# Kernel optimization log

Hardware: AMD Instinct MI355X
Metric: run time of the kernel (lower is better)

The kernel has to match this reference:

```python
import jax, jax.numpy as jnp
import numpy as np
import math

CHANNELS = 512
N_HEADS = 8
K_CH = CHANNELS // N_HEADS            # 64 per-head dim
ROPE_D = int(K_CH * 0.5)              # 32 dims get RoPE, rest pass through
BASE = 10000


def _rope(x):
    # x: [b, h, t, dk]; rotate first ROPE_D dims (half-split style, matching the torch module)
    d = ROPE_D
    t = x.shape[2]
    theta = 1.0 / (BASE ** (jnp.arange(0, d, 2, dtype=jnp.float32) / d))      # [d/2]
    ang = jnp.arange(t, dtype=jnp.float32)[:, None] * theta[None, :]          # [t, d/2]
    ang = jnp.concatenate([ang, ang], axis=-1)                                # [t, d]
    cos = jnp.cos(ang)[None, None, :, :].astype(x.dtype)
    sin = jnp.sin(ang)[None, None, :, :].astype(x.dtype)
    x_rope, x_pass = x[..., :d], x[..., d:]
    neg_half = jnp.concatenate([-x_rope[..., d // 2:], x_rope[..., :d // 2]], axis=-1)
    return jnp.concatenate([x_rope * cos + neg_half * sin, x_pass], axis=-1)


def _split_heads(y):
    # [b, (h c), t] -> [b, h, t, c]
    b, _, t = y.shape
    return y.reshape(b, N_HEADS, K_CH, t).transpose(0, 1, 3, 2)


def setup_inputs() -> dict:
    key = jax.random.key(0)
    ks = jax.random.split(key, 10)
    B, T = 8, 1024
    w_scale = 1.0 / math.sqrt(CHANNELS)
    return {
        "x": jax.random.normal(ks[0], (B, CHANNELS, T), jnp.float32),
        "c": jax.random.normal(ks[1], (B, CHANNELS, T), jnp.float32),
        "Wq": jax.random.normal(ks[2], (CHANNELS, CHANNELS), jnp.float32) * w_scale,
        "bq": jax.random.normal(ks[3], (CHANNELS,), jnp.float32) * 0.02,
        "Wk": jax.random.normal(ks[4], (CHANNELS, CHANNELS), jnp.float32) * w_scale,
        "bk": jax.random.normal(ks[5], (CHANNELS,), jnp.float32) * 0.02,
        "Wv": jax.random.normal(ks[6], (CHANNELS, CHANNELS), jnp.float32) * w_scale,
        "bv": jax.random.normal(ks[7], (CHANNELS,), jnp.float32) * 0.02,
        "Wo": jax.random.normal(ks[8], (CHANNELS, CHANNELS), jnp.float32) * w_scale,
        "bo": jax.random.normal(ks[9], (CHANNELS,), jnp.float32) * 0.02,
    }


def reference(x, c, Wq, bq, Wk, bk, Wv, bv, Wo, bo):
    # 1x1 Conv1d == per-timestep linear over channels
    q = jnp.einsum('oc,bct->bot', Wq, x) + bq[None, :, None]
    k = jnp.einsum('oc,bct->bot', Wk, c) + bk[None, :, None]
    v = jnp.einsum('oc,bct->bot', Wv, c) + bv[None, :, None]

    q = _rope(_split_heads(q))            # [b,h,t,ck]
    k = _rope(_split_heads(k))            # [b,h,s,ck]
    v = _split_heads(v)                   # [b,h,s,ck]

    scale = 1.0 / math.sqrt(K_CH)
    scores = jnp.einsum('bhtc,bhsc->bhts', q, k) * scale
    p_attn = jax.nn.softmax(scores, axis=-1)       # dropout p=0 -> identity
    out = jnp.einsum('bhts,bhsc->bhtc', p_attn, v)

    b, _, t, _ = out.shape
    out = out.transpose(0, 1, 3, 2).reshape(b, CHANNELS, t)   # [b, (h c), t]
    return jnp.einsum('oc,bct->bot', Wo, out) + bo[None, :, None]
```

## Files before the change

### kernel.cpp

```cpp
#include <hip/hip_runtime.h>

typedef __bf16 bf16x8 __attribute__((ext_vector_type(8)));
typedef float  f32x4  __attribute__((ext_vector_type(4)));

__device__ __forceinline__ unsigned short f2bf(float f){
    union { float f; unsigned u; } v; v.f = f;
    v.u += 0x7fffu + ((v.u >> 16) & 1u);
    return (unsigned short)(v.u >> 16);
}
__device__ __forceinline__ unsigned short f2bf_trunc(float f){
    union { float f; unsigned u; } v; v.f = f;
    return (unsigned short)(v.u >> 16);
}
__device__ __forceinline__ void gl2lds16(const unsigned short* g, unsigned short* l){
    __builtin_amdgcn_global_load_lds(
        (const __attribute__((address_space(1))) void*)g,
        (__attribute__((address_space(3))) void*)l, 16, 0, 0);
}

__global__ __launch_bounds__(256) void cvt_bf16_4(const float* __restrict__ w0, const float* __restrict__ w1,
                                                  const float* __restrict__ w2, const float* __restrict__ w3,
                                                  unsigned short* __restrict__ o0, unsigned short* __restrict__ o1,
                                                  unsigned short* __restrict__ o2, unsigned short* __restrict__ o3){
    const float* in; unsigned short* out;
    switch (blockIdx.y){
        case 0: in = w0; out = o0; break;
        case 1: in = w1; out = o1; break;
        case 2: in = w2; out = o2; break;
        default: in = w3; out = o3; break;
    }
    int i = (blockIdx.x * 256 + threadIdx.x) * 4;
    float4 v = *(const float4*)(in + i);
    ushort4 o; o.x = f2bf(v.x); o.y = f2bf(v.y); o.z = f2bf(v.z); o.w = f2bf(v.w);
    *(ushort4*)(out + i) = o;
}

__global__ __launch_bounds__(256) void transpose_cvt(const float* __restrict__ x, const float* __restrict__ c,
                                                     unsigned short* __restrict__ xt, unsigned short* __restrict__ ct){
    __shared__ float tile[64][72];
    const int z = blockIdx.z;
    const float* in = (z < 8) ? x : c;
    unsigned short* out = (z < 8) ? xt : ct;
    const int b = z & 7;
    const int t0 = blockIdx.x * 64, c0 = blockIdx.y * 64;
    const int tid = threadIdx.x;
    {
        int r = tid >> 2, q = (tid & 3) * 16;
        const float* src = in + ((size_t)b * 512 + c0 + r) * 1024 + t0 + q;
        *(float4*)&tile[r][q + 0]  = ((const float4*)src)[0];
        *(float4*)&tile[r][q + 4]  = ((const float4*)src)[1];
        *(float4*)&tile[r][q + 8]  = ((const float4*)src)[2];
        *(float4*)&tile[r][q + 12] = ((const float4*)src)[3];
    }
    __syncthreads();
    {
        int tr = tid >> 2, cj = (tid & 3) * 16;
        unsigned pw[8];
        #pragma unroll
        for (int j = 0; j < 8; j++){
            unsigned lo = f2bf(tile[cj + 2*j    ][tr]);
            unsigned hi = f2bf(tile[cj + 2*j + 1][tr]);
            pw[j] = lo | (hi << 16);
        }
        unsigned short* dst = out + ((size_t)b * 1024 + t0 + tr) * 512 + c0 + cj;
        uint4 o0 = {pw[0], pw[1], pw[2], pw[3]};
        uint4 o1 = {pw[4], pw[5], pw[6], pw[7]};
        ((uint4*)dst)[0] = o0;
        ((uint4*)dst)[1] = o1;
    }
}

__device__ __forceinline__ void gemm_mainloop(const unsigned short* __restrict__ A,
                                              const unsigned short* __restrict__ Bm,
                                              unsigned short* a_s, unsigned short* b_s,
                                              int m0, int n0, int tid, f32x4 acc[4][4]){
    const int wave = tid >> 6, lane = tid & 63;
    const int l15 = lane & 15, l4 = lane >> 4;
    const int mw = (wave >> 1) * 64, nw = (wave & 1) * 64;
    const int r8 = lane >> 3, c8l = lane & 7;
    const int csw = (c8l ^ r8) * 8;
    const int rp = l15 & 7;

    for (int k0 = 0; k0 < 512; k0 += 64){
        #pragma unroll
        for (int i = 0; i < 4; i++){
            int rg = i * 4 + wave;
            int row = rg * 8 + r8;
            gl2lds16(A  + (size_t)(m0 + row) * 512 + k0 + csw, a_s + rg * 512);
            gl2lds16(Bm + (size_t)(n0 + row) * 512 + k0 + csw, b_s + rg * 512);
        }
        __syncthreads();
        #pragma unroll
        for (int kk = 0; kk < 2; kk++){
            bf16x8 af[4], bfr[4];
            #pragma unroll
            for (int mt = 0; mt < 4; mt++)
                af[mt] = *(const bf16x8*)&a_s[(mw + mt*16 + l15)*64 + (((kk*4) + l4) ^ rp)*8];
            #pragma unroll
            for (int ct = 0; ct < 4; ct++)
                bfr[ct] = *(const bf16x8*)&b_s[(nw + ct*16 + l15)*64 + (((kk*4) + l4) ^ rp)*8];
            #pragma unroll
            for (int mt = 0; mt < 4; mt++)
                #pragma unroll
                for (int ct = 0; ct < 4; ct++)
                    acc[mt][ct] = __builtin_amdgcn_mfma_f32_16x16x32_bf16(
                        af[mt], bfr[ct], acc[mt][ct], 0, 0, 0);
        }
        __syncthreads();
    }
}

__global__ __launch_bounds__(256) void qkv_gemm(const unsigned short* __restrict__ xt,
                                                const unsigned short* __restrict__ ct,
                                                const unsigned short* __restrict__ wq,
                                                const unsigned short* __restrict__ wk,
                                                const unsigned short* __restrict__ wv,
                                                const float* __restrict__ bq_,
                                                const float* __restrict__ bk_,
                                                const float* __restrict__ bv_,
                                                unsigned short* __restrict__ qt,
                                                unsigned short* __restrict__ kt,
                                                unsigned short* __restrict__ vct){
    __shared__ unsigned short a_s[128*64];
    __shared__ unsigned short b_s[128*64];
    const int z = blockIdx.y, bid = blockIdx.x;
    const unsigned short *A, *Bm;
    int m0, n0;
    if (z == 0){ A = xt; Bm = wq; m0 = (bid >> 2)*128; n0 = (bid & 3)*128; }
    else if (z == 1){ A = ct; Bm = wk; m0 = (bid >> 2)*128; n0 = (bid & 3)*128; }
    else { A = wv; Bm = ct; m0 = (bid & 3)*128; n0 = (bid >> 2)*128; }
    const int tid = threadIdx.x;
    const int wave = tid >> 6, lane = tid & 63;
    const int l15 = lane & 15, l4 = lane >> 4;
    const int mw = (wave >> 1) * 64, nw = (wave & 1) * 64;
    const f32x4 vzero = {0.f, 0.f, 0.f, 0.f};
    f32x4 acc[4][4];
    #pragma unroll
    for (int i = 0; i < 4; i++)
        #pragma unroll
        for (int j = 0; j < 4; j++) acc[i][j] = vzero;

    gemm_mainloop(A, Bm, a_s, b_s, m0, n0, tid, acc);

    if (z < 2){
        unsigned short* out = (z == 0) ? qt : kt;
        const float* bias = (z == 0) ? bq_ : bk_;
        const float oscale = (z == 0) ? 0.125f : 1.0f;
        float bv4[4];
        #pragma unroll
        for (int ct2 = 0; ct2 < 4; ct2++) bv4[ct2] = bias[n0 + nw + ct2*16 + l15];
        const float theta = __powf(10000.0f, -(float)l15 * (1.0f / 16.0f));
        #pragma unroll
        for (int mt = 0; mt < 4; mt++){
            #pragma unroll
            for (int r = 0; r < 4; r++){
                int row = m0 + mw + mt*16 + l4*4 + r;
                int t = row & 1023;
                float v[4];
                #pragma unroll
                for (int ct2 = 0; ct2 < 4; ct2++) v[ct2] = acc[mt][ct2][r] + bv4[ct2];
                float sn, cn;
                __sincosf((float)t * theta, &sn, &cn);
                float r0 = v[0] * cn - v[1] * sn;
                float r1 = v[1] * cn + v[0] * sn;
                v[0] = r0; v[1] = r1;
                #pragma unroll
                for (int ct2 = 0; ct2 < 4; ct2++)
                    out[(size_t)row * 512 + n0 + nw + ct2*16 + l15] = f2bf(v[ct2] * oscale);
            }
        }
    } else {
        #pragma unroll
        for (int mt = 0; mt < 4; mt++){
            #pragma unroll
            for (int r = 0; r < 4; r++){
                int row = m0 + mw + mt*16 + l4*4 + r;
                float bb = bv_[row];
                #pragma unroll
                for (int ct2 = 0; ct2 < 4; ct2++){
                    int n = n0 + nw + ct2*16 + l15;
                    size_t oaddr = (size_t)(n >> 10) * 524288 + (size_t)row * 1024 + (n & 1023);
                    vct[oaddr] = f2bf(acc[mt][ct2][r] + bb);
                }
            }
        }
    }
}

__global__ __launch_bounds__(256) void gemm_o(const unsigned short* __restrict__ wo,
                                              const unsigned short* __restrict__ attnT,
                                              const float* __restrict__ bo,
                                              float* __restrict__ out){
    __shared__ unsigned short a_s[128*64];
    __shared__ unsigned short b_s[128*64];
    const int m0 = blockIdx.x * 128, n0 = blockIdx.y * 128;
    const int tid = threadIdx.x;
    const int wave = tid >> 6, lane = tid & 63;
    const int l15 = lane & 15, l4 = lane >> 4;
    const int mw = (wave >> 1) * 64, nw = (wave & 1) * 64;
    const f32x4 vzero = {0.f, 0.f, 0.f, 0.f};
    f32x4 acc[4][4];
    #pragma unroll
    for (int i = 0; i < 4; i++)
        #pragma unroll
        for (int j = 0; j < 4; j++) acc[i][j] = vzero;

    gemm_mainloop(wo, attnT, a_s, b_s, m0, n0, tid, acc);

    #pragma unroll
    for (int mt = 0; mt < 4; mt++){
        #pragma unroll
        for (int r = 0; r < 4; r++){
            int row = m0 + mw + mt*16 + l4*4 + r;
            float bb = bo[row];
            #pragma unroll
            for (int ct2 = 0; ct2 < 4; ct2++){
                int n = n0 + nw + ct2*16 + l15;
                size_t oaddr = (size_t)(n >> 10) * 524288 + (size_t)row * 1024 + (n & 1023);
                out[oaddr] = acc[mt][ct2][r] + bb;
            }
        }
    }
}

__global__ __launch_bounds__(256, 2) void flash_attn(const unsigned short* __restrict__ qt,
                                                     const unsigned short* __restrict__ kt,
                                                     const unsigned short* __restrict__ vct,
                                                     unsigned short* __restrict__ attnT){
    __shared__ unsigned short k_s[2][64*64];
    __shared__ unsigned short v_s[2][64*64];
    __shared__ unsigned short p_s[4][16][72];
    const int bh = blockIdx.y, b = bh >> 3, h = bh & 7;
    const int q0 = blockIdx.x * 128;
    const int tid = threadIdx.x, wave = tid >> 6, lane = tid & 63;
    const int l15 = lane & 15, l4 = lane >> 4;
    const int r8 = lane >> 3, c8l = lane & 7;
    const int csw = (c8l ^ r8) * 8;
    const int rp = l15 & 7;
    const f32x4 vzero = {0.f, 0.f, 0.f, 0.f};

    const unsigned short* kbase = kt  + (size_t)(b*1024)*512 + h*64;
    const unsigned short* vbase = vct + (size_t)(b*512 + h*64)*1024;

    bf16x8 qf[2][2];
    #pragma unroll
    for (int st = 0; st < 2; st++)
        #pragma unroll
        for (int kh = 0; kh < 2; kh++)
            qf[st][kh] = *(const bf16x8*)(qt + (size_t)(b*1024 + q0 + wave*32 + st*16 + l15)*512
                                             + h*64 + kh*32 + l4*8);

    f32x4 o_acc[2][4], l_acc[2];
    #pragma unroll
    for (int st = 0; st < 2; st++){
        l_acc[st] = vzero;
        #pragma unroll
        for (int dt = 0; dt < 4; dt++) o_acc[st][dt] = vzero;
    }
    const __bf16 one_bf = (__bf16)1.0f;
    const bf16x8 ones = {one_bf, one_bf, one_bf, one_bf, one_bf, one_bf, one_bf, one_bf};

    auto stage = [&](int tile, int buf){
        const int s0n = tile * 64;
        #pragma unroll
        for (int i = 0; i < 2; i++){
            int rg = i * 4 + wave;
            int row = rg * 8 + r8;
            gl2lds16(kbase + (size_t)(s0n + row)*512 + csw, &k_s[buf][rg*512]);
            gl2lds16(vbase + (size_t)row*1024 + s0n + csw, &v_s[buf][rg*512]);
        }
    };

    stage(0, 0);
    __syncthreads();

    for (int it = 0; it < 16; ++it){
        const int cur = it & 1;
        if (it < 15) stage(it + 1, cur ^ 1);

        bf16x8 kf[2][4], vf[2][4];
        #pragma unroll
        for (int kh = 0; kh < 2; kh++)
            #pragma unroll
            for (int ct = 0; ct < 4; ct++)
                kf[kh][ct] = *(const bf16x8*)&k_s[cur][(ct*16 + l15)*64 + ((kh*4 + l4) ^ rp)*8];
        #pragma unroll
        for (int sh = 0; sh < 2; sh++)
            #pragma unroll
            for (int dt = 0; dt < 4; dt++)
                vf[sh][dt] = *(const bf16x8*)&v_s[cur][(dt*16 + l15)*64 + ((sh*4 + l4) ^ rp)*8];

        #pragma unroll
        for (int st = 0; st < 2; st++){
            f32x4 sa[4];
            #pragma unroll
            for (int ct = 0; ct < 4; ct++) sa[ct] = vzero;
            #pragma unroll
            for (int kh = 0; kh < 2; kh++)
                #pragma unroll
                for (int ct = 0; ct < 4; ct++)
                    sa[ct] = __builtin_amdgcn_mfma_f32_16x16x32_bf16(qf[st][kh], kf[kh][ct], sa[ct], 0, 0, 0);
            #pragma unroll
            for (int ct = 0; ct < 4; ct++)
                #pragma unroll
                for (int r = 0; r < 4; r++)
                    sa[ct][r] = __expf(sa[ct][r]);
            #pragma unroll
            for (int ct = 0; ct < 4; ct++)
                #pragma unroll
                for (int r = 0; r < 4; r++)
                    p_s[wave][l4*4 + r][ct*16 + l15] = f2bf_trunc(sa[ct][r]);
            bf16x8 ap0 = *(const bf16x8*)&p_s[wave][l15][l4*8];
            bf16x8 ap1 = *(const bf16x8*)&p_s[wave][l15][32 + l4*8];
            l_acc[st] = __builtin_amdgcn_mfma_f32_16x16x32_bf16(ap0, ones, l_acc[st], 0, 0, 0);
            l_acc[st] = __builtin_amdgcn_mfma_f32_16x16x32_bf16(ap1, ones, l_acc[st], 0, 0, 0);
            #pragma unroll
            for (int dt = 0; dt < 4; dt++){
                o_acc[st][dt] = __builtin_amdgcn_mfma_f32_16x16x32_bf16(ap0, vf[0][dt], o_acc[st][dt], 0, 0, 0);
                o_acc[st][dt] = __builtin_amdgcn_mfma_f32_16x16x32_bf16(ap1, vf[1][dt], o_acc[st][dt], 0, 0, 0);
            }
        }
        __syncthreads();
    }

    #pragma unroll
    for (int st = 0; st < 2; st++){
        float rl[4];
        #pragma unroll
        for (int r = 0; r < 4; r++) rl[r] = __builtin_amdgcn_rcpf(l_acc[st][r]);
        #pragma unroll
        for (int dt = 0; dt < 4; dt++)
            #pragma unroll
            for (int r = 0; r < 4; r++){
                int row = q0 + wave*32 + st*16 + l4*4 + r;
                attnT[(size_t)(b*1024 + row)*512 + h*64 + dt*16 + l15] = f2bf(o_acc[st][dt][r] * rl[r]);
            }
    }
}

extern "C" void kernel_launch(void* const* d_in, const int* in_sizes, int n_in,
                              void* d_out, int out_size, void* d_ws, size_t ws_size,
                              hipStream_t stream){
    const float* x  = (const float*)d_in[0];
    const float* c  = (const float*)d_in[1];
    const float* Wq = (const float*)d_in[2];
    const float* bq = (const float*)d_in[3];
    const float* Wk = (const float*)d_in[4];
    const float* bk = (const float*)d_in[5];
    const float* Wv = (const float*)d_in[6];
    const float* bv = (const float*)d_in[7];
    const float* Wo = (const float*)d_in[8];
    const float* bo = (const float*)d_in[9];

    unsigned short* wq_b = (unsigned short*)d_ws;
    unsigned short* wk_b = wq_b + 262144;
    unsigned short* wv_b = wk_b + 262144;
    unsigned short* wo_b = wv_b + 262144;
    unsigned short* xt   = wo_b + 262144;
    unsigned short* ct   = xt  + 4194304;
    unsigned short* qt   = ct  + 4194304;
    unsigned short* kt   = qt  + 4194304;
    unsigned short* vct  = kt  + 4194304;
    unsigned short* attnT = xt;

    cvt_bf16_4<<<dim3(256, 4), 256, 0, stream>>>(Wq, Wk, Wv, Wo, wq_b, wk_b, wv_b, wo_b);
    transpose_cvt<<<dim3(16, 8, 16), 256, 0, stream>>>(x, c, xt, ct);
    qkv_gemm<<<dim3(256, 3), 256, 0, stream>>>(xt, ct, wq_b, wk_b, wv_b, bq, bk, bv, qt, kt, vct);
    flash_attn<<<dim3(8, 64), 256, 0, stream>>>(qt, kt, vct, attnT);
    gemm_o<<<dim3(4, 64), 256, 0, stream>>>(wo_b, attnT, bo, (float*)d_out);
}
```

Measured before the change: 172.9 us.

## Fuse weight conversion into transpose kernel, shrink gemm_o tile, use exp2 softmax

```diff
diff --git a/kernel.cpp b/kernel.cpp
--- a/kernel.cpp
+++ b/kernel.cpp
@@ -18,27 +18,32 @@
         (__attribute__((address_space(3))) void*)l, 16, 0, 0);
 }
 
-__global__ __launch_bounds__(256) void cvt_bf16_4(const float* __restrict__ w0, const float* __restrict__ w1,
-                                                  const float* __restrict__ w2, const float* __restrict__ w3,
-                                                  unsigned short* __restrict__ o0, unsigned short* __restrict__ o1,
-                                                  unsigned short* __restrict__ o2, unsigned short* __restrict__ o3){
-    const float* in; unsigned short* out;
-    switch (blockIdx.y){
-        case 0: in = w0; out = o0; break;
-        case 1: in = w1; out = o1; break;
-        case 2: in = w2; out = o2; break;
-        default: in = w3; out = o3; break;
-    }
-    int i = (blockIdx.x * 256 + threadIdx.x) * 4;
-    float4 v = *(const float4*)(in + i);
-    ushort4 o; o.x = f2bf(v.x); o.y = f2bf(v.y); o.z = f2bf(v.z); o.w = f2bf(v.w);
-    *(ushort4*)(out + i) = o;
-}
-
 __global__ __launch_bounds__(256) void transpose_cvt(const float* __restrict__ x, const float* __restrict__ c,
-                                                     unsigned short* __restrict__ xt, unsigned short* __restrict__ ct){
+                                                     const float* __restrict__ w0, const float* __restrict__ w1,
+                                                     const float* __restrict__ w2, const float* __restrict__ w3,
+                                                     unsigned short* __restrict__ xt, unsigned short* __restrict__ ct,
+                                                     unsigned short* __restrict__ o0, unsigned short* __restrict__ o1,
+                                                     unsigned short* __restrict__ o2, unsigned short* __restrict__ o3){
     __shared__ float tile[64][72];
     const int z = blockIdx.z;
+    if (z == 16){
+        int fid = (blockIdx.x * 8 + blockIdx.y) * 256 + threadIdx.x;
+        const float* in; unsigned short* out;
+        switch (fid >> 13){
+            case 0: in = w0; out = o0; break;
+            case 1: in = w1; out = o1; break;
+            case 2: in = w2; out = o2; break;
+            default: in = w3; out = o3; break;
+        }
+        int off = (fid & 8191) * 32;
+        #pragma unroll
+        for (int j = 0; j < 8; j++){
+            float4 v = *(const float4*)(in + off + j*4);
+            ushort4 o; o.x = f2bf(v.x); o.y = f2bf(v.y); o.z = f2bf(v.z); o.w = f2bf(v.w);
+            *(ushort4*)(out + off + j*4) = o;
+        }
+        return;
+    }
     const float* in = (z < 8) ? x : c;
     unsigned short* out = (z < 8) ? xt : ct;
     const int b = z & 7;
@@ -63,10 +68,10 @@
             pw[j] = lo | (hi << 16);
         }
         unsigned short* dst = out + ((size_t)b * 1024 + t0 + tr) * 512 + c0 + cj;
-        uint4 o0 = {pw[0], pw[1], pw[2], pw[3]};
-        uint4 o1 = {pw[4], pw[5], pw[6], pw[7]};
-        ((uint4*)dst)[0] = o0;
-        ((uint4*)dst)[1] = o1;
+        uint4 q0 = {pw[0], pw[1], pw[2], pw[3]};
+        uint4 q1 = {pw[4], pw[5], pw[6], pw[7]};
+        ((uint4*)dst)[0] = q0;
+        ((uint4*)dst)[1] = q1;
     }
 }
 
@@ -145,7 +150,7 @@
     if (z < 2){
         unsigned short* out = (z == 0) ? qt : kt;
         const float* bias = (z == 0) ? bq_ : bk_;
-        const float oscale = (z == 0) ? 0.125f : 1.0f;
+        const float oscale = (z == 0) ? 0.1803368801111137f : 1.0f;
         float bv4[4];
         #pragma unroll
         for (int ct2 = 0; ct2 < 4; ct2++) bv4[ct2] = bias[n0 + nw + ct2*16 + l15];
@@ -191,30 +196,60 @@
                                               const unsigned short* __restrict__ attnT,
                                               const float* __restrict__ bo,
                                               float* __restrict__ out){
-    __shared__ unsigned short a_s[128*64];
+    __shared__ unsigned short a_s[64*64];
     __shared__ unsigned short b_s[128*64];
-    const int m0 = blockIdx.x * 128, n0 = blockIdx.y * 128;
+    const int m0 = blockIdx.x * 64, n0 = blockIdx.y * 128;
     const int tid = threadIdx.x;
     const int wave = tid >> 6, lane = tid & 63;
     const int l15 = lane & 15, l4 = lane >> 4;
-    const int mw = (wave >> 1) * 64, nw = (wave & 1) * 64;
+    const int nw = wave * 32;
+    const int r8 = lane >> 3, c8l = lane & 7;
+    const int csw = (c8l ^ r8) * 8;
+    const int rp = l15 & 7;
     const f32x4 vzero = {0.f, 0.f, 0.f, 0.f};
-    f32x4 acc[4][4];
-    #pragma unroll
-    for (int i = 0; i < 4; i++)
-        #pragma unroll
-        for (int j = 0; j < 4; j++) acc[i][j] = vzero;
-
-    gemm_mainloop(wo, attnT, a_s, b_s, m0, n0, tid, acc);
+    f32x4 acc[4][2];
+    #pragma unroll
+    for (int i = 0; i < 4; i++){ acc[i][0] = vzero; acc[i][1] = vzero; }
+
+    for (int k0 = 0; k0 < 512; k0 += 64){
+        #pragma unroll
+        for (int i = 0; i < 2; i++){
+            int rg = wave * 2 + i;
+            gl2lds16(wo + (size_t)(m0 + rg*8 + r8) * 512 + k0 + csw, a_s + rg * 512);
+        }
+        #pragma unroll
+        for (int i = 0; i < 4; i++){
+            int rg = wave * 4 + i;
+            gl2lds16(attnT + (size_t)(n0 + rg*8 + r8) * 512 + k0 + csw, b_s + rg * 512);
+        }
+        __syncthreads();
+        #pragma unroll
+        for (int kk = 0; kk < 2; kk++){
+            bf16x8 af[4], bfr[2];
+            #pragma unroll
+            for (int mt = 0; mt < 4; mt++)
+                af[mt] = *(const bf16x8*)&a_s[(mt*16 + l15)*64 + (((kk*4) + l4) ^ rp)*8];
+            #pragma unroll
+            for (int ct = 0; ct < 2; ct++)
+                bfr[ct] = *(const bf16x8*)&b_s[(nw + ct*16 + l15)*64 + (((kk*4) + l4) ^ rp)*8];
+            #pragma unroll
+            for (int mt = 0; mt < 4; mt++)
+                #pragma unroll
+                for (int ct = 0; ct < 2; ct++)
+                    acc[mt][ct] = __builtin_amdgcn_mfma_f32_16x16x32_bf16(
+                        af[mt], bfr[ct], acc[mt][ct], 0, 0, 0);
+        }
+        __syncthreads();
+    }
 
     #pragma unroll
     for (int mt = 0; mt < 4; mt++){
         #pragma unroll
         for (int r = 0; r < 4; r++){
-            int row = m0 + mw + mt*16 + l4*4 + r;
+            int row = m0 + mt*16 + l4*4 + r;
             float bb = bo[row];
             #pragma unroll
-            for (int ct2 = 0; ct2 < 4; ct2++){
+            for (int ct2 = 0; ct2 < 2; ct2++){
                 int n = n0 + nw + ct2*16 + l15;
                 size_t oaddr = (size_t)(n >> 10) * 524288 + (size_t)row * 1024 + (n & 1023);
                 out[oaddr] = acc[mt][ct2][r] + bb;
@@ -304,7 +339,7 @@
             for (int ct = 0; ct < 4; ct++)
                 #pragma unroll
                 for (int r = 0; r < 4; r++)
-                    sa[ct][r] = __expf(sa[ct][r]);
+                    sa[ct][r] = exp2f(sa[ct][r]);
             #pragma unroll
             for (int ct = 0; ct < 4; ct++)
                 #pragma unroll
@@ -363,9 +398,9 @@
     unsigned short* vct  = kt  + 4194304;
     unsigned short* attnT = xt;
 
-    cvt_bf16_4<<<dim3(256, 4), 256, 0, stream>>>(Wq, Wk, Wv, Wo, wq_b, wk_b, wv_b, wo_b);
-    transpose_cvt<<<dim3(16, 8, 16), 256, 0, stream>>>(x, c, xt, ct);
+    transpose_cvt<<<dim3(16, 8, 17), 256, 0, stream>>>(x, c, Wq, Wk, Wv, Wo,
+                                                       xt, ct, wq_b, wk_b, wv_b, wo_b);
     qkv_gemm<<<dim3(256, 3), 256, 0, stream>>>(xt, ct, wq_b, wk_b, wv_b, bq, bk, bv, qt, kt, vct);
     flash_attn<<<dim3(8, 64), 256, 0, stream>>>(qt, kt, vct, attnT);
-    gemm_o<<<dim3(4, 64), 256, 0, stream>>>(wo_b, attnT, bo, (float*)d_out);
-}
+    gemm_o<<<dim3(8, 64), 256, 0, stream>>>(wo_b, attnT, bo, (float*)d_out);
+}
```

After: 171.6 us. No clear change (-0.7%).
